# Kernel tuning notes

Hardware: AMD Instinct MI355X
Metric: run time of the kernel (lower is better)

Reference implementation:

```python
import jax, jax.numpy as jnp
import numpy as np

N = 40000      # nodes
E = 640000     # edges
D = 128        # embed_dim
H = 8          # heads
DH = D // H    # per-head dim
L = 3          # n_layers
IN = 64        # in_dim
FF = 218       # embed_dim2 (ffn hidden)
OUT = 1        # out_dim
EPS = 1e-5
NEG_SLOPE = 0.2


def setup_inputs() -> dict:
    key = jax.random.key(0)
    ks = jax.random.split(key, 16)
    nrm = lambda k, shape, s=0.1: (jax.random.normal(k, shape, jnp.float32) * s)
    return {
        "x": jax.random.normal(ks[0], (N, IN), jnp.float32),
        "src": jax.random.randint(ks[1], (E,), 0, N, jnp.int32),
        "dst": jax.random.randint(ks[2], (E,), 0, N, jnp.int32),
        "W_emb": nrm(ks[3], (IN, D)),
        "b_emb": jnp.zeros((D,), jnp.float32),
        "gat_W": nrm(ks[4], (L, D, D)),
        "attn_l": nrm(ks[5], (L, H, DH)),
        "attn_r": nrm(ks[6], (L, H, DH)),
        "gat_b": jnp.zeros((L, D), jnp.float32),
        "bn1_g": jnp.ones((L, D), jnp.float32),
        "bn1_b": jnp.zeros((L, D), jnp.float32),
        "ff_W1": nrm(ks[7], (L, D, FF)),
        "ff_b1": jnp.zeros((L, FF), jnp.float32),
        "ff_W2": nrm(ks[8], (L, FF, D)),
        "ff_b2": jnp.zeros((L, D), jnp.float32),
        "bn2_g": jnp.ones((L, D), jnp.float32),
        "bn2_b": jnp.zeros((L, D), jnp.float32),
        "dec_W1": nrm(ks[9], ((L + 1) * D, D)),
        "dec_bn_g": jnp.ones((D,), jnp.float32),
        "dec_bn_b": jnp.zeros((D,), jnp.float32),
        "dec_W2": nrm(ks[10], (D, OUT)),
    }


def _batchnorm(h, g, b):
    # BatchNorm1d in training mode: batch stats over nodes, biased variance
    mu = h.mean(axis=0)
    var = h.var(axis=0)
    return g * (h - mu) * jax.lax.rsqrt(var + EPS) + b


def _gat_layer(h, src, dst, W, al, ar, bias):
    n = h.shape[0]
    feat = (h @ W).reshape(n, H, DH)                      # [N,H,DH]
    el = (feat * al).sum(-1)                               # [N,H]
    er = (feat * ar).sum(-1)                               # [N,H]
    e = jax.nn.leaky_relu(el[src] + er[dst], NEG_SLOPE)    # [E,H]
    # segment softmax over incoming edges of each dst node
    emax = jax.ops.segment_max(e, dst, num_segments=n)
    ex = jnp.exp(e - emax[dst])
    den = jax.ops.segment_sum(ex, dst, num_segments=n)
    alpha = ex / den[dst]                                  # [E,H]
    msg = alpha[:, :, None] * feat[src]                    # [E,H,DH]
    out = jax.ops.segment_sum(msg, dst, num_segments=n)    # [N,H,DH]
    out = out + bias.reshape(H, DH)
    return out.reshape(n, D)


def reference(x, src, dst, W_emb, b_emb, gat_W, attn_l, attn_r, gat_b,
              bn1_g, bn1_b, ff_W1, ff_b1, ff_W2, ff_b2, bn2_g, bn2_b,
              dec_W1, dec_bn_g, dec_bn_b, dec_W2):
    h = x @ W_emb + b_emb                                  # embed_layer
    xs = [h]
    for l in range(L):
        # message passing with skip connection
        h = h + _gat_layer(h, src, dst, gat_W[l], attn_l[l], attn_r[l], gat_b[l])
        # feed forward: BN -> Skip(Linear,ReLU,Linear) -> BN
        h = _batchnorm(h, bn1_g[l], bn1_b[l])
        y = jax.nn.relu(h @ ff_W1[l] + ff_b1[l]) @ ff_W2[l] + ff_b2[l]
        h = _batchnorm(h + y, bn2_g[l], bn2_b[l])
        xs.append(h)
    h = jnp.concatenate(xs, axis=-1)                       # JumpingKnowledge 'cat'
    # decision MLP: relu(BN(h W1)) W2, no biases
    h = jax.nn.relu(_batchnorm(h @ dec_W1, dec_bn_g, dec_bn_b))
    return h @ dec_W2
```

## Files before the change

### kernel.cpp

```cpp
#include <hip/hip_runtime.h>
#include <hip/hip_bf16.h>
#include <math.h>

#define N_NODES 40000
#define N_EDGES 640000
#define DIM     128
#define HEADS   8
#define DHEAD   16
#define LAYERS  3
#define IN_DIM  64
#define FF_DIM  218
#define BN_EPS  1e-5f
#define NEG_SLOPE 0.2f
#define INV_N   (1.f / N_NODES)
#define NREP    64

typedef __attribute__((ext_vector_type(8))) short  bhalf8;
typedef __attribute__((ext_vector_type(4))) float  floatx4;
typedef __attribute__((ext_vector_type(4))) int    intx4;

__device__ __forceinline__ unsigned bfpack2(float a, float b) {
    unsigned ua = __float_as_uint(a);
    ua = ua + 0x7FFFu + ((ua >> 16) & 1u);
    unsigned ub = __float_as_uint(b);
    ub = ub + 0x7FFFu + ((ub >> 16) & 1u);
    return (ua >> 16) | (ub & 0xFFFF0000u);
}
__device__ __forceinline__ unsigned short bf16of(float a) {
    unsigned ua = __float_as_uint(a);
    ua = ua + 0x7FFFu + ((ua >> 16) & 1u);
    return (unsigned short)(ua >> 16);
}
__device__ __forceinline__ float bf2f(unsigned short u) {
    return __uint_as_float(((unsigned)u) << 16);
}
__device__ __forceinline__ float bflo(unsigned u) { return __uint_as_float(u << 16); }
__device__ __forceinline__ float bfhi(unsigned u) { return __uint_as_float(u & 0xFFFF0000u); }
__device__ __forceinline__ float rsum16(float v) {
    v += __shfl_xor(v, 1, 16);
    v += __shfl_xor(v, 2, 16);
    v += __shfl_xor(v, 4, 16);
    v += __shfl_xor(v, 8, 16);
    return v;
}

#define OFF_EMB 0
#define OFF_GAT 8192
#define OFF_W1  57344
#define OFF_W2  143360
#define OFF_DEC 229376
#define WPK_TOT 294912

__global__ void pack_weights_kernel(const float* __restrict__ W_emb,
                                    const float* __restrict__ gat_W,
                                    const float* __restrict__ ff_W1,
                                    const float* __restrict__ ff_W2,
                                    const float* __restrict__ dec_W1,
                                    unsigned short* __restrict__ wpk) {
    int i = blockIdx.x * 256 + threadIdx.x;
    if (i >= WPK_TOT) return;
    int o = i;
    if (o < 8192) {
        int n = o >> 6, k = o & 63;
        wpk[OFF_EMB + o] = bf16of(W_emb[k * 128 + n]);
        return;
    }
    o -= 8192;
    if (o < 3 * 16384) {
        int l = o >> 14, r = o & 16383;
        int n = r >> 7, k = r & 127;
        wpk[OFF_GAT + o] = bf16of(gat_W[l * 16384 + k * 128 + n]);
        return;
    }
    o -= 3 * 16384;
    if (o < 3 * 28672) {
        int l = o / 28672, r = o % 28672;
        int n = r >> 7, k = r & 127;
        float v = (n < FF_DIM) ? ff_W1[(size_t)l * 128 * FF_DIM + k * FF_DIM + n] : 0.f;
        wpk[OFF_W1 + o] = bf16of(v);
        return;
    }
    o -= 3 * 28672;
    if (o < 3 * 28672) {
        int l = o / 28672, r = o % 28672;
        int n = r / 224, k = r % 224;
        float v = (k < FF_DIM) ? ff_W2[(size_t)l * FF_DIM * 128 + k * 128 + n] : 0.f;
        wpk[OFF_W2 + o] = bf16of(v);
        return;
    }
    o -= 3 * 28672;
    {
        int n = o >> 9, k = o & 511;
        wpk[OFF_DEC + o] = bf16of(dec_W1[k * 128 + n]);
    }
}

__global__ void hist_kernel(const int* __restrict__ dst, int* __restrict__ counts) {
    int e = blockIdx.x * blockDim.x + threadIdx.x;
    if (e < N_EDGES) atomicAdd(&counts[dst[e]], 1);
}

__global__ __launch_bounds__(1024) void scan_kernel(const int* __restrict__ counts,
                                                    int* __restrict__ indptr,
                                                    int* __restrict__ cursor, int n) {
    __shared__ int tsum[1024];
    const int CH = 40;
    int tid = threadIdx.x;
    int base = tid * CH;
    int loc[CH];
    int s = 0;
    #pragma unroll
    for (int i = 0; i < CH; i++) {
        int idx = base + i;
        int v = (idx < n) ? counts[idx] : 0;
        loc[i] = s;
        s += v;
    }
    tsum[tid] = s;
    __syncthreads();
    for (int offs = 1; offs < 1024; offs <<= 1) {
        int t = (tid >= offs) ? tsum[tid - offs] : 0;
        __syncthreads();
        tsum[tid] += t;
        __syncthreads();
    }
    int carry = (tid > 0) ? tsum[tid - 1] : 0;
    #pragma unroll
    for (int i = 0; i < CH; i++) {
        int idx = base + i;
        if (idx < n) {
            int v = carry + loc[i];
            indptr[idx] = v;
            cursor[idx] = v;
        }
    }
    if (tid == 1023) indptr[n] = tsum[1023];
}

__global__ void scatter_kernel(const int* __restrict__ src, const int* __restrict__ dst,
                               int* __restrict__ cursor,
                               int* __restrict__ srcs_csr) {
    int e = blockIdx.x * blockDim.x + threadIdx.x;
    if (e < N_EDGES) {
        int d = dst[e];
        int pos = atomicAdd(&cursor[d], 1);
        srcs_csr[pos] = src[e];
    }
}

template<int NT, int KPAD, int AMODE, bool ABF16, int MT, bool ELER, bool RESBF>
__global__ __launch_bounds__(256) void gemm_l2_kernel(
    const float* __restrict__ A, const unsigned short* __restrict__ Abf, int lda,
    const unsigned short* __restrict__ Bpk,
    const float* __restrict__ bias,
    const void* __restrict__ resv, int ldres,
    const float* __restrict__ res_stats, const float* __restrict__ res_g,
    const float* __restrict__ res_b,
    float* __restrict__ C, unsigned short* __restrict__ Cbf, int ldc,
    float* __restrict__ out_stats,
    int M, int Nact, int relu,
    const float* __restrict__ a_stats, float* __restrict__ a_stats_out,
    const float* __restrict__ a_g, const float* __restrict__ a_b,
    const float* __restrict__ al, const float* __restrict__ ar,
    float* __restrict__ el_out, float* __restrict__ er_out)
{
    constexpr int SCN = (AMODE > 0) ? KPAD : 1;
    constexpr int BROWS = 64 * MT;
    constexpr int STEPS = KPAD / 32;
    constexpr int CST = (STEPS > 2) ? 2 : STEPS;
    __shared__ float sc_s[SCN];
    __shared__ float sh_s[SCN];
    __shared__ float st_sum[128];
    __shared__ float st_sq[128];
    __shared__ float el_s[ELER ? BROWS : 1][ELER ? NT : 1];
    __shared__ float er_s[ELER ? BROWS : 1][ELER ? NT : 1];

    int tid = threadIdx.x, wave = tid >> 6, lane = tid & 63;
    int q = lane >> 4, tl = lane & 15;
    int colbase = blockIdx.y * (NT * 16);
    int row0b = blockIdx.x * BROWS;
    int rowtile = row0b + wave * (MT * 16);

    if constexpr (AMODE == 1 || AMODE == 2) {
        for (int idx = tid; idx < KPAD; idx += 256) {
            float scv = 1.f, shv = 0.f;
            if constexpr (AMODE == 1) {
                float mu = a_stats[idx] * INV_N;
                float var = a_stats[128 + idx] * INV_N - mu * mu;
                scv = a_g[idx] * rsqrtf(var + BN_EPS);
                shv = a_b[idx] - mu * scv;
            } else {
                int l = idx >> 7;
                if (l > 0) {
                    int c = idx & 127;
                    const float* st = a_stats + (l - 1) * 256;
                    float mu = st[c] * INV_N;
                    float var = st[128 + c] * INV_N - mu * mu;
                    scv = a_g[(l - 1) * 128 + c] * rsqrtf(var + BN_EPS);
                    shv = a_b[(l - 1) * 128 + c] - mu * scv;
                }
            }
            sc_s[idx] = scv;
            sh_s[idx] = shv;
        }
        __syncthreads();
    }
    if constexpr (AMODE == 3) {
        for (int idx = tid; idx < 128; idx += 256) {
            float s = 0.f, sq = 0.f;
            #pragma unroll 8
            for (int r = 0; r < NREP; r++) {
                s  += a_stats[r * 256 + idx];
                sq += a_stats[r * 256 + 128 + idx];
            }
            a_stats_out[idx] = s;
            a_stats_out[128 + idx] = sq;
            float mu = s * INV_N;
            float var = sq * INV_N - mu * mu;
            float scv = a_g[idx] * rsqrtf(var + BN_EPS);
            sc_s[idx] = scv;
            sh_s[idx] = a_b[idx] - mu * scv;
        }
        __syncthreads();
    }

    int rowm[MT];
    bool vrm[MT];
    #pragma unroll
    for (int mt = 0; mt < MT; mt++) {
        rowm[mt] = rowtile + mt * 16 + tl;
        vrm[mt] = rowm[mt] < M;
    }
    const unsigned short* bp = Bpk + (size_t)colbase * KPAD;

    floatx4 acc[MT][NT] = {};

    #pragma unroll
    for (int c0 = 0; c0 < STEPS; c0 += CST) {
        intx4  arawb[CST][MT];
        floatx4 araw0[ABF16 ? 1 : CST][ABF16 ? 1 : MT];
        floatx4 araw1[ABF16 ? 1 : CST][ABF16 ? 1 : MT];
        bhalf8 breg[CST][NT];
        #pragma unroll
        for (int cs = 0; cs < CST; cs++) {
            if (c0 + cs >= STEPS) continue;
            int gk = (c0 + cs) * 32 + q * 8;
            #pragma unroll
            for (int j = 0; j < NT; j++)
                breg[cs][j] = *(const bhalf8*)(bp + (size_t)(j * 16 + tl) * KPAD + gk);
            #pragma unroll
            for (int mt = 0; mt < MT; mt++) {
                if constexpr (ABF16) {
                    intx4 u = {};
                    if (vrm[mt]) u = *(const intx4*)(Abf + (size_t)rowm[mt] * lda + gk);
                    arawb[cs][mt] = u;
                } else {
                    floatx4 x0 = {}, x1 = {};
                    if (vrm[mt]) {
                        const float* ap = A + (size_t)rowm[mt] * lda + gk;
                        x0 = *(const floatx4*)ap;
                        x1 = *(const floatx4*)(ap + 4);
                    }
                    araw0[cs][mt] = x0;
                    araw1[cs][mt] = x1;
                }
            }
        }
        #pragma unroll
        for (int cs = 0; cs < CST; cs++) {
            if (c0 + cs >= STEPS) continue;
            int gk = (c0 + cs) * 32 + q * 8;
            bhalf8 af[MT];
            #pragma unroll
            for (int mt = 0; mt < MT; mt++) {
                if constexpr (ABF16) {
                    intx4 u = arawb[cs][mt];
                    if constexpr (AMODE > 0) {
                        #pragma unroll
                        for (int w = 0; w < 4; w++) {
                            unsigned uw = (unsigned)u[w];
                            float lo = bflo(uw), hi = bfhi(uw);
                            lo = fmaf(sc_s[gk + 2 * w],     lo, sh_s[gk + 2 * w]);
                            hi = fmaf(sc_s[gk + 2 * w + 1], hi, sh_s[gk + 2 * w + 1]);
                            u[w] = (int)bfpack2(lo, hi);
                        }
                    }
                    af[mt] = *(bhalf8*)&u;
                } else {
                    floatx4 x0 = araw0[cs][mt], x1 = araw1[cs][mt];
                    if constexpr (AMODE > 0) {
                        #pragma unroll
                        for (int jj = 0; jj < 4; jj++) {
                            x0[jj] = fmaf(sc_s[gk + jj],     x0[jj], sh_s[gk + jj]);
                            x1[jj] = fmaf(sc_s[gk + 4 + jj], x1[jj], sh_s[gk + 4 + jj]);
                        }
                    }
                    intx4 t = intx4{(int)bfpack2(x0[0], x0[1]), (int)bfpack2(x0[2], x0[3]),
                                    (int)bfpack2(x1[0], x1[1]), (int)bfpack2(x1[2], x1[3])};
                    af[mt] = *(bhalf8*)&t;
                }
            }
            #pragma unroll
            for (int mt = 0; mt < MT; mt++)
                #pragma unroll
                for (int j = 0; j < NT; j++)
                    acc[mt][j] = __builtin_amdgcn_mfma_f32_16x16x32_bf16(af[mt], breg[cs][j], acc[mt][j], 0, 0, 0);
        }
    }

    float psum[NT], psq[NT];
    #pragma unroll
    for (int j = 0; j < NT; j++) { psum[j] = 0.f; psq[j] = 0.f; }

    #pragma unroll
    for (int j = 0; j < NT; j++) {
        int c = colbase + j * 16 + tl;
        bool cok = c < Nact;
        float bv = (bias && cok) ? bias[c] : 0.f;
        float rsc = 1.f, rsh = 0.f;
        if (res_stats && cok) {
            float mu = res_stats[c] * INV_N;
            float var = res_stats[128 + c] * INV_N - mu * mu;
            rsc = res_g[c] * rsqrtf(var + BN_EPS);
            rsh = res_b[c] - mu * rsc;
        }
        float alc = 0.f, arc = 0.f;
        if constexpr (ELER) { alc = al[c]; arc = ar[c]; }
        #pragma unroll
        for (int mt = 0; mt < MT; mt++) {
            #pragma unroll
            for (int reg = 0; reg < 4; reg++) {
                int r = rowtile + mt * 16 + q * 4 + reg;
                bool rok = r < M;
                float v = 0.f;
                if (rok && cok) {
                    v = acc[mt][j][reg] + bv;
                    if (resv) {
                        size_t ri = (size_t)r * ldres + c;
                        float rv = RESBF ? bf2f(((const unsigned short*)resv)[ri])
                                         : ((const float*)resv)[ri];
                        v = fmaf(rsc, rv, v + rsh);
                    }
                    if (relu) v = fmaxf(v, 0.f);
                    if (out_stats) { psum[j] += v; psq[j] = fmaf(v, v, psq[j]); }
                }
                if constexpr (ELER) {
                    float pel = rsum16(v * alc);
                    float per_ = rsum16(v * arc);
                    if (tl == 0) {
                        int rl = wave * (MT * 16) + mt * 16 + q * 4 + reg;
                        el_s[rl][j] = pel;
                        er_s[rl][j] = per_;
                    }
                }
                if (rok) {
                    if (Cbf) Cbf[(size_t)r * ldc + c] = bf16of(v);
                    else if (cok) C[(size_t)r * ldc + c] = v;
                }
            }
        }
    }

    if constexpr (ELER) {
        __syncthreads();
        int gh = blockIdx.y * NT;
        for (int idx = tid; idx < BROWS * NT; idx += 256) {
            int rl = idx / NT, hj = idx % NT;
            int r = row0b + rl;
            if (r < M) {
                el_out[(size_t)r * 8 + gh + hj] = el_s[rl][hj];
                er_out[(size_t)r * 8 + gh + hj] = er_s[rl][hj];
            }
        }
    }

    if (out_stats) {
        __syncthreads();
        if (tid < 128) { st_sum[tid] = 0.f; st_sq[tid] = 0.f; }
        __syncthreads();
        #pragma unroll
        for (int j = 0; j < NT; j++) {
            int c = colbase + j * 16 + tl;
            if (c < 128) { atomicAdd(&st_sum[c], psum[j]); atomicAdd(&st_sq[c], psq[j]); }
        }
        __syncthreads();
        if (tid < 128) {
            atomicAdd(&out_stats[tid], st_sum[tid]);
            atomicAdd(&out_stats[128 + tid], st_sq[tid]);
        }
    }
}

__global__ __launch_bounds__(256) void gat_aggregate_kernel(
    const unsigned short* __restrict__ feat,
    const float* __restrict__ el, const float* __restrict__ er,
    const int* __restrict__ indptr, const int* __restrict__ srcs_csr,
    const unsigned short* __restrict__ h_in, int ldh,
    const float* __restrict__ hstats, const float* __restrict__ hg,
    const float* __restrict__ hb,
    const float* __restrict__ bias,
    unsigned short* __restrict__ outp,
    float* __restrict__ stats_rep)
{
    int n = blockIdx.x;
    int t = threadIdx.x;
    int p = t >> 6;
    int lane = t & 63;
    int d0 = lane * 2;
    int hh = lane >> 3;
    int pick = lane & 3;
    int gb = lane & 56;
    __shared__ float red[4][128];
    __shared__ float denh[4][HEADS];
    int beg = indptr[n], end = indptr[n + 1];
    float ern = er[(size_t)n * 8 + hh];

    float acc0 = 0.f, acc1 = 0.f, den = 0.f;
    int i = beg + p;
    for (; i + 12 < end; i += 16) {
        int s0 = srcs_csr[i],     s1 = srcs_csr[i + 4];
        int s2 = srcs_csr[i + 8], s3 = srcs_csr[i + 12];
        int sp = pick == 0 ? s0 : pick == 1 ? s1 : pick == 2 ? s2 : s3;
        float ee = el[(size_t)sp * 8 + hh] + ern;
        unsigned f0 = *(const unsigned*)(feat + (size_t)s0 * DIM + d0);
        unsigned f1 = *(const unsigned*)(feat + (size_t)s1 * DIM + d0);
        unsigned f2 = *(const unsigned*)(feat + (size_t)s2 * DIM + d0);
        unsigned f3 = *(const unsigned*)(feat + (size_t)s3 * DIM + d0);
        float aa = expf(ee > 0.f ? ee : NEG_SLOPE * ee);
        float a0 = __shfl(aa, gb + 0);
        float a1 = __shfl(aa, gb + 1);
        float a2 = __shfl(aa, gb + 2);
        float a3 = __shfl(aa, gb + 3);
        den += (a0 + a1) + (a2 + a3);
        acc0 = fmaf(a0, bflo(f0), acc0); acc1 = fmaf(a0, bfhi(f0), acc1);
        acc0 = fmaf(a1, bflo(f1), acc0); acc1 = fmaf(a1, bfhi(f1), acc1);
        acc0 = fmaf(a2, bflo(f2), acc0); acc1 = fmaf(a2, bfhi(f2), acc1);
        acc0 = fmaf(a3, bflo(f3), acc0); acc1 = fmaf(a3, bfhi(f3), acc1);
    }
    for (; i < end; i += 4) {
        int s0 = srcs_csr[i];
        float e0 = el[(size_t)s0 * 8 + hh] + ern;
        unsigned f0 = *(const unsigned*)(feat + (size_t)s0 * DIM + d0);
        float a0 = expf(e0 > 0.f ? e0 : NEG_SLOPE * e0);
        den += a0;
        acc0 = fmaf(a0, bflo(f0), acc0);
        acc1 = fmaf(a0, bfhi(f0), acc1);
    }
    red[p][d0] = acc0;
    red[p][d0 + 1] = acc1;
    if ((lane & 7) == 0) denh[p][hh] = den;
    __syncthreads();
    if (t < 128) {
        int d = t, h = d >> 4;
        float tot = (red[0][d] + red[1][d]) + (red[2][d] + red[3][d]);
        float dtot = (denh[0][h] + denh[1][h]) + (denh[2][h] + denh[3][h]);
        float inv = dtot > 0.f ? 1.f / dtot : 0.f;
        float hv = bf2f(h_in[(size_t)n * ldh + d]);
        if (hstats) {
            float mu = hstats[d] * INV_N;
            float var = hstats[128 + d] * INV_N - mu * mu;
            float s = hg[d] * rsqrtf(var + BN_EPS);
            hv = fmaf(s, hv - mu, hb[d]);
        }
        unsigned short ub = bf16of(hv + tot * inv + bias[d]);
        outp[(size_t)n * DIM + d] = ub;
        float vr = bf2f(ub);
        float* rep = stats_rep + ((size_t)(n & (NREP - 1)) << 8);
        atomicAdd(&rep[d], vr);
        atomicAdd(&rep[128 + d], vr * vr);
    }
}

__global__ __launch_bounds__(256) void decide_kernel(
    const unsigned short* __restrict__ z, const float* __restrict__ stats,
    const float* __restrict__ g, const float* __restrict__ b,
    const float* __restrict__ W2, float* __restrict__ outp, int M)
{
    int wid = threadIdx.x >> 6, lane = threadIdx.x & 63;
    int n = blockIdx.x * 4 + wid;
    if (n >= M) return;
    float acc = 0.f;
    #pragma unroll
    for (int cc = 0; cc < 2; cc++) {
        int c = lane + cc * 64;
        float mu  = stats[c] * INV_N;
        float var = stats[DIM + c] * INV_N - mu * mu;
        float v = fmaf(g[c] * rsqrtf(var + BN_EPS), bf2f(z[(size_t)n * DIM + c]) - mu, b[c]);
        v = fmaxf(v, 0.f);
        acc = fmaf(v, W2[c], acc);
    }
    #pragma unroll
    for (int offs = 32; offs > 0; offs >>= 1)
        acc += __shfl_down(acc, offs);
    if (lane == 0) outp[n] = acc;
}

extern "C" void kernel_launch(void* const* d_in, const int* in_sizes, int n_in,
                              void* d_out, int out_size, void* d_ws, size_t ws_size,
                              hipStream_t stream)
{
    const float* x      = (const float*)d_in[0];
    const int*   src    = (const int*)  d_in[1];
    const int*   dst    = (const int*)  d_in[2];
    const float* W_emb  = (const float*)d_in[3];
    const float* b_emb  = (const float*)d_in[4];
    const float* gat_W  = (const float*)d_in[5];
    const float* attn_l = (const float*)d_in[6];
    const float* attn_r = (const float*)d_in[7];
    const float* gat_b  = (const float*)d_in[8];
    const float* bn1_g  = (const float*)d_in[9];
    const float* bn1_b  = (const float*)d_in[10];
    const float* ff_W1  = (const float*)d_in[11];
    const float* ff_b1  = (const float*)d_in[12];
    const float* ff_W2  = (const float*)d_in[13];
    const float* ff_b2  = (const float*)d_in[14];
    const float* bn2_g  = (const float*)d_in[15];
    const float* bn2_b  = (const float*)d_in[16];
    const float* dec_W1 = (const float*)d_in[17];
    const float* dec_bn_g = (const float*)d_in[18];
    const float* dec_bn_b = (const float*)d_in[19];
    const float* dec_W2 = (const float*)d_in[20];
    float* outp = (float*)d_out;

    char* ws = (char*)d_ws;
    size_t off = 0;
    auto alloc = [&](size_t bytes) -> void* {
        void* p = ws + off;
        off += (bytes + 255) & ~(size_t)255;
        return p;
    };
    unsigned short* xsb = (unsigned short*)alloc((size_t)N_NODES * 512 * 2);
    unsigned short* zb  = (unsigned short*)alloc((size_t)N_NODES * DIM * 2);
    unsigned short* featb = (unsigned short*)alloc((size_t)N_NODES * DIM * 2);
    float* el    = (float*)alloc((size_t)N_NODES * HEADS * 4);
    float* er    = (float*)alloc((size_t)N_NODES * HEADS * 4);
    unsigned short* y1b = (unsigned short*)alloc((size_t)N_NODES * 224 * 2);
    unsigned short* btb = (unsigned short*)alloc((size_t)N_NODES * DIM * 2);
    int*   counts= (int*)  alloc((size_t)N_NODES * 4);
    float* statsAll = (float*)alloc((3 * NREP * 256 + 7 * 256) * 4);
    unsigned short* wpk = (unsigned short*)alloc((size_t)WPK_TOT * 2);
    int*   indptr= (int*)  alloc((size_t)(N_NODES + 1) * 4);
    int*   cursor= (int*)  alloc((size_t)N_NODES * 4);
    int*   srcs_csr = (int*)alloc((size_t)N_EDGES * 4);
    (void)ws_size; (void)in_sizes; (void)n_in; (void)out_size;

    float* rep1   = statsAll;
    float* stats1c= statsAll + 3 * NREP * 256;
    float* stats2 = statsAll + 3 * NREP * 256 + 3 * 256;
    float* statsD = statsAll + 3 * NREP * 256 + 6 * 256;

    dim3 gg2((N_NODES + 127) / 128, 2);

    hipMemsetAsync(counts, 0, (size_t)N_NODES * 4 + (size_t)(3 * NREP * 256 + 7 * 256) * 4, stream);
    hist_kernel<<<(N_EDGES + 255) / 256, 256, 0, stream>>>(dst, counts);
    scan_kernel<<<1, 1024, 0, stream>>>(counts, indptr, cursor, N_NODES);
    scatter_kernel<<<(N_EDGES + 255) / 256, 256, 0, stream>>>(src, dst, cursor, srcs_csr);
    pack_weights_kernel<<<(WPK_TOT + 255) / 256, 256, 0, stream>>>(
        W_emb, gat_W, ff_W1, ff_W2, dec_W1, wpk);

    gemm_l2_kernel<4, 64, 0, false, 2, false, false><<<gg2, 256, 0, stream>>>(
        x, nullptr, IN_DIM, wpk + OFF_EMB, b_emb,
        nullptr, 0, nullptr, nullptr, nullptr,
        nullptr, xsb, 512, nullptr,
        N_NODES, DIM, 0, nullptr, nullptr, nullptr, nullptr,
        nullptr, nullptr, nullptr, nullptr);

    for (int l = 0; l < LAYERS; l++) {
        const unsigned short* h_cur = xsb + (size_t)l * DIM;
        const float* hstats = l ? stats2 + (l - 1) * 256 : nullptr;
        const float* hg = l ? bn2_g + (l - 1) * DIM : nullptr;
        const float* hb = l ? bn2_b + (l - 1) * DIM : nullptr;
        if (l == 0)
            gemm_l2_kernel<4, 128, 0, true, 2, true, false><<<gg2, 256, 0, stream>>>(
                nullptr, h_cur, 512, wpk + OFF_GAT + l * 16384, nullptr,
                nullptr, 0, nullptr, nullptr, nullptr,
                nullptr, featb, DIM, nullptr,
                N_NODES, DIM, 0, nullptr, nullptr, nullptr, nullptr,
                attn_l + l * DIM, attn_r + l * DIM, el, er);
        else
            gemm_l2_kernel<4, 128, 1, true, 2, true, false><<<gg2, 256, 0, stream>>>(
                nullptr, h_cur, 512, wpk + OFF_GAT + l * 16384, nullptr,
                nullptr, 0, nullptr, nullptr, nullptr,
                nullptr, featb, DIM, nullptr,
                N_NODES, DIM, 0, hstats, nullptr, hg, hb,
                attn_l + l * DIM, attn_r + l * DIM, el, er);
        gat_aggregate_kernel<<<N_NODES, 256, 0, stream>>>(
            featb, el, er, indptr, srcs_csr, h_cur, 512,
            hstats, hg, hb, gat_b + l * DIM, btb,
            rep1 + (size_t)l * NREP * 256);
        gemm_l2_kernel<7, 128, 3, true, 2, false, false><<<gg2, 256, 0, stream>>>(
            nullptr, btb, DIM, wpk + OFF_W1 + l * 28672,
            ff_b1 + l * FF_DIM,
            nullptr, 0, nullptr, nullptr, nullptr,
            nullptr, y1b, 224, nullptr,
            N_NODES, FF_DIM, 1,
            rep1 + (size_t)l * NREP * 256, stats1c + l * 256,
            bn1_g + l * DIM, bn1_b + l * DIM,
            nullptr, nullptr, nullptr, nullptr);
        gemm_l2_kernel<4, 224, 0, true, 2, false, true><<<gg2, 256, 0, stream>>>(
            nullptr, y1b, 224, wpk + OFF_W2 + l * 28672,
            ff_b2 + l * DIM,
            btb, DIM, stats1c + l * 256, bn1_g + l * DIM, bn1_b + l * DIM,
            nullptr, xsb + (size_t)(l + 1) * DIM, 512, stats2 + l * 256,
            N_NODES, DIM, 0, nullptr, nullptr, nullptr, nullptr,
            nullptr, nullptr, nullptr, nullptr);
    }

    gemm_l2_kernel<4, 512, 2, true, 2, false, false><<<gg2, 256, 0, stream>>>(
        nullptr, xsb, 512, wpk + OFF_DEC, nullptr,
        nullptr, 0, nullptr, nullptr, nullptr,
        nullptr, zb, DIM, statsD,
        N_NODES, DIM, 0, stats2, nullptr, bn2_g, bn2_b,
        nullptr, nullptr, nullptr, nullptr);
    decide_kernel<<<(N_NODES + 3) / 4, 256, 0, stream>>>(
        zb, statsD, dec_bn_g, dec_bn_b, dec_W2, outp, N_NODES);
}
```

Before: 787.8 us.

## Map one wavefront per destination node in GAT aggregation with shared-memory stats

The GAT aggregation kernel now assigns one 64-lane wavefront per destination node, with four nodes per block, instead of splitting one node's edges across four wavefronts and reducing them through shared memory. Batch-norm sum and sum-of-squares are first accumulated in shared memory per block, and only then atomically added to the global replicated stats. This cuts the number of blocks and global atomics by about a factor of four and removes the cross-wave reduction step. In exchange, each node's edge loop runs serially within a single wavefront, which gives less memory-level parallelism per node.

```diff
diff --git a/kernel.cpp b/kernel.cpp
--- a/kernel.cpp
+++ b/kernel.cpp
@@ -402,72 +402,82 @@
     unsigned short* __restrict__ outp,
     float* __restrict__ stats_rep)
 {
-    int n = blockIdx.x;
     int t = threadIdx.x;
-    int p = t >> 6;
+    int ln = t >> 6;
+    int n = blockIdx.x * 4 + ln;
     int lane = t & 63;
     int d0 = lane * 2;
     int hh = lane >> 3;
     int pick = lane & 3;
     int gb = lane & 56;
-    __shared__ float red[4][128];
-    __shared__ float denh[4][HEADS];
-    int beg = indptr[n], end = indptr[n + 1];
-    float ern = er[(size_t)n * 8 + hh];
-
-    float acc0 = 0.f, acc1 = 0.f, den = 0.f;
-    int i = beg + p;
-    for (; i + 12 < end; i += 16) {
-        int s0 = srcs_csr[i],     s1 = srcs_csr[i + 4];
-        int s2 = srcs_csr[i + 8], s3 = srcs_csr[i + 12];
-        int sp = pick == 0 ? s0 : pick == 1 ? s1 : pick == 2 ? s2 : s3;
-        float ee = el[(size_t)sp * 8 + hh] + ern;
-        unsigned f0 = *(const unsigned*)(feat + (size_t)s0 * DIM + d0);
-        unsigned f1 = *(const unsigned*)(feat + (size_t)s1 * DIM + d0);
-        unsigned f2 = *(const unsigned*)(feat + (size_t)s2 * DIM + d0);
-        unsigned f3 = *(const unsigned*)(feat + (size_t)s3 * DIM + d0);
-        float aa = expf(ee > 0.f ? ee : NEG_SLOPE * ee);
-        float a0 = __shfl(aa, gb + 0);
-        float a1 = __shfl(aa, gb + 1);
-        float a2 = __shfl(aa, gb + 2);
-        float a3 = __shfl(aa, gb + 3);
-        den += (a0 + a1) + (a2 + a3);
-        acc0 = fmaf(a0, bflo(f0), acc0); acc1 = fmaf(a0, bfhi(f0), acc1);
-        acc0 = fmaf(a1, bflo(f1), acc0); acc1 = fmaf(a1, bfhi(f1), acc1);
-        acc0 = fmaf(a2, bflo(f2), acc0); acc1 = fmaf(a2, bfhi(f2), acc1);
-        acc0 = fmaf(a3, bflo(f3), acc0); acc1 = fmaf(a3, bfhi(f3), acc1);
-    }
-    for (; i < end; i += 4) {
-        int s0 = srcs_csr[i];
-        float e0 = el[(size_t)s0 * 8 + hh] + ern;
-        unsigned f0 = *(const unsigned*)(feat + (size_t)s0 * DIM + d0);
-        float a0 = expf(e0 > 0.f ? e0 : NEG_SLOPE * e0);
-        den += a0;
-        acc0 = fmaf(a0, bflo(f0), acc0);
-        acc1 = fmaf(a0, bfhi(f0), acc1);
-    }
-    red[p][d0] = acc0;
-    red[p][d0 + 1] = acc1;
-    if ((lane & 7) == 0) denh[p][hh] = den;
+    __shared__ float stats_s[2][128];
+    if (t < 128) { stats_s[0][t] = 0.f; stats_s[1][t] = 0.f; }
+    __syncthreads();
+
+    if (n < N_NODES) {
+        int beg = indptr[n], end = indptr[n + 1];
+        float ern = er[(size_t)n * 8 + hh];
+
+        float acc0 = 0.f, acc1 = 0.f, den = 0.f;
+        int i = beg;
+        for (; i + 3 < end; i += 4) {
+            int s0 = srcs_csr[i],     s1 = srcs_csr[i + 1];
+            int s2 = srcs_csr[i + 2], s3 = srcs_csr[i + 3];
+            int sp = pick == 0 ? s0 : pick == 1 ? s1 : pick == 2 ? s2 : s3;
+            float ee = el[(size_t)sp * 8 + hh] + ern;
+            unsigned f0 = *(const unsigned*)(feat + (size_t)s0 * DIM + d0);
+            unsigned f1 = *(const unsigned*)(feat + (size_t)s1 * DIM + d0);
+            unsigned f2 = *(const unsigned*)(feat + (size_t)s2 * DIM + d0);
+            unsigned f3 = *(const unsigned*)(feat + (size_t)s3 * DIM + d0);
+            float aa = expf(ee > 0.f ? ee : NEG_SLOPE * ee);
+            float a0 = __shfl(aa, gb + 0);
+            float a1 = __shfl(aa, gb + 1);
+            float a2 = __shfl(aa, gb + 2);
+            float a3 = __shfl(aa, gb + 3);
+            den += (a0 + a1) + (a2 + a3);
+            acc0 = fmaf(a0, bflo(f0), acc0); acc1 = fmaf(a0, bfhi(f0), acc1);
+            acc0 = fmaf(a1, bflo(f1), acc0); acc1 = fmaf(a1, bfhi(f1), acc1);
+            acc0 = fmaf(a2, bflo(f2), acc0); acc1 = fmaf(a2, bfhi(f2), acc1);
+            acc0 = fmaf(a3, bflo(f3), acc0); acc1 = fmaf(a3, bfhi(f3), acc1);
+        }
+        for (; i < end; i++) {
+            int s0 = srcs_csr[i];
+            float e0 = el[(size_t)s0 * 8 + hh] + ern;
+            unsigned f0 = *(const unsigned*)(feat + (size_t)s0 * DIM + d0);
+            float a0 = expf(e0 > 0.f ? e0 : NEG_SLOPE * e0);
+            den += a0;
+            acc0 = fmaf(a0, bflo(f0), acc0);
+            acc1 = fmaf(a0, bfhi(f0), acc1);
+        }
+        float inv = den > 0.f ? 1.f / den : 0.f;
+
+        unsigned hu = *(const unsigned*)(h_in + (size_t)n * ldh + d0);
+        float hv0 = bflo(hu), hv1 = bfhi(hu);
+        if (hstats) {
+            float mu0 = hstats[d0] * INV_N;
+            float var0 = hstats[128 + d0] * INV_N - mu0 * mu0;
+            float s0 = hg[d0] * rsqrtf(var0 + BN_EPS);
+            hv0 = fmaf(s0, hv0 - mu0, hb[d0]);
+            float mu1 = hstats[d0 + 1] * INV_N;
+            float var1 = hstats[128 + d0 + 1] * INV_N - mu1 * mu1;
+            float s1 = hg[d0 + 1] * rsqrtf(var1 + BN_EPS);
+            hv1 = fmaf(s1, hv1 - mu1, hb[d0 + 1]);
+        }
+        unsigned short u0 = bf16of(hv0 + acc0 * inv + bias[d0]);
+        unsigned short u1 = bf16of(hv1 + acc1 * inv + bias[d0 + 1]);
+        *(unsigned*)(outp + (size_t)n * DIM + d0) =
+            (unsigned)u0 | ((unsigned)u1 << 16);
+        float v0 = bf2f(u0), v1 = bf2f(u1);
+        atomicAdd(&stats_s[0][d0],     v0);
+        atomicAdd(&stats_s[1][d0],     v0 * v0);
+        atomicAdd(&stats_s[0][d0 + 1], v1);
+        atomicAdd(&stats_s[1][d0 + 1], v1 * v1);
+    }
     __syncthreads();
     if (t < 128) {
-        int d = t, h = d >> 4;
-        float tot = (red[0][d] + red[1][d]) + (red[2][d] + red[3][d]);
-        float dtot = (denh[0][h] + denh[1][h]) + (denh[2][h] + denh[3][h]);
-        float inv = dtot > 0.f ? 1.f / dtot : 0.f;
-        float hv = bf2f(h_in[(size_t)n * ldh + d]);
-        if (hstats) {
-            float mu = hstats[d] * INV_N;
-            float var = hstats[128 + d] * INV_N - mu * mu;
-            float s = hg[d] * rsqrtf(var + BN_EPS);
-            hv = fmaf(s, hv - mu, hb[d]);
-        }
-        unsigned short ub = bf16of(hv + tot * inv + bias[d]);
-        outp[(size_t)n * DIM + d] = ub;
-        float vr = bf2f(ub);
-        float* rep = stats_rep + ((size_t)(n & (NREP - 1)) << 8);
-        atomicAdd(&rep[d], vr);
-        atomicAdd(&rep[128 + d], vr * vr);
+        float* rep = stats_rep + ((size_t)(blockIdx.x & (NREP - 1)) << 8);
+        atomicAdd(&rep[t], stats_s[0][t]);
+        atomicAdd(&rep[128 + t], stats_s[1][t]);
     }
 }
 
@@ -584,7 +594,7 @@
                 nullptr, featb, DIM, nullptr,
                 N_NODES, DIM, 0, hstats, nullptr, hg, hb,
                 attn_l + l * DIM, attn_r + l * DIM, el, er);
-        gat_aggregate_kernel<<<N_NODES, 256, 0, stream>>>(
+        gat_aggregate_kernel<<<(N_NODES + 3) / 4, 256, 0, stream>>>(
             featb, el, er, indptr, srcs_csr, h_cur, 512,
             hstats, hg, hb, gat_b + l * DIM, btb,
             rep1 + (size_t)l * NREP * 256);
```

New measurement: 801.5 us. No clear change (+1.7%).
